# Kernel tuning notes

Measured on AMD Instinct MI355X. Metric: run time of the kernel, lower is better.

The kernel has to match this reference:

```python
import jax, jax.numpy as jnp
import numpy as np

N, E, G = 100000, 600000, 64  # nodes, edges, graphs
F_IN, W, EPS = 32, 128, 1e-5


def setup_inputs() -> dict:
    key = jax.random.key(0)
    ks = jax.random.split(key, 16)
    p = lambda k, shape: jax.random.normal(k, shape, dtype=jnp.float32) * 0.1
    z = lambda n: jnp.zeros((n,), jnp.float32)
    o = lambda n: jnp.ones((n,), jnp.float32)
    return {
        "x": jax.random.normal(ks[0], (N, F_IN), dtype=jnp.float32),
        "edge_index": jax.random.randint(ks[1], (2, E), 0, N, dtype=jnp.int32),
        "batch": jnp.sort(jax.random.randint(ks[2], (N,), 0, G, dtype=jnp.int32)),
        # GCNConv layers
        "W1": p(ks[3], (F_IN, W)), "b1": z(W),
        "W2": p(ks[4], (W, W)), "b2": z(W),
        # mlp_first: Linear -> BN -> ReLU -> Linear
        "W3": p(ks[5], (W, W)), "b3": z(W), "g1": o(W), "be1": z(W),
        "W4": p(ks[6], (W, W)), "b4": z(W),
        # mlp: Linear -> BN -> ReLU -> Linear
        "W5": p(ks[7], (W, W // 2)), "b5": z(W // 2), "g2": o(W // 2), "be2": z(W // 2),
        "W6": p(ks[8], (W // 2, 1)), "b6": z(1),
    }


def gcn_conv(x, src, dst, Wt, b):
    # PyG GCNConv with add_self_loops=True: D^-1/2 (A+I) D^-1/2 (x W) + b
    h = x @ Wt  # [N, width]
    deg = jax.ops.segment_sum(jnp.ones(src.shape[0], x.dtype), dst, num_segments=N) + 1.0
    dinv = jax.lax.rsqrt(deg)
    norm = dinv[src] * dinv[dst]  # per-edge normalization
    agg = jax.ops.segment_sum(h[src] * norm[:, None], dst, num_segments=N)
    # self-loop term: norm for (i,i) is 1/deg[i]
    return agg + h * (dinv * dinv)[:, None] + b


def batch_norm(x, g, b):
    # training-mode BatchNorm1d (batch stats, biased var)
    mu = x.mean(axis=0)
    var = jnp.mean((x - mu) ** 2, axis=0)
    return (x - mu) * jax.lax.rsqrt(var + EPS) * g + b


def reference(x, edge_index, batch, W1, b1, W2, b2, W3, b3, g1, be1, W4, b4, W5, b5, g2, be2, W6, b6):
    src, dst = edge_index[0], edge_index[1]
    x = jax.nn.relu(gcn_conv(x, src, dst, W1, b1))
    x = jax.nn.relu(gcn_conv(x, src, dst, W2, b2))
    # mlp_first + ReLU
    x = jax.nn.relu(batch_norm(x @ W3 + b3, g1, be1)) @ W4 + b4
    x = jax.nn.relu(x)
    # global max pool over nodes per graph
    x = jax.ops.segment_max(x, batch, num_segments=G)  # [G, width]
    # final mlp
    x = jax.nn.relu(batch_norm(x @ W5 + b5, g2, be2)) @ W6 + b6
    return x[:, 0]
```

## Files before the change

kernel.cpp:

```cpp
#include <hip/hip_runtime.h>

#define N_NODES 100000
#define N_EDGES 600000
#define N_GRAPHS 64
#define EPS 1e-5f
#define SCAN_BLOCKS 391

typedef unsigned short u16;
typedef unsigned int u32;
typedef __attribute__((ext_vector_type(8))) short bf16x8;
typedef __attribute__((ext_vector_type(4))) float f32x4;

__device__ __forceinline__ float bf2f(u16 u) { return __uint_as_float(((u32)u) << 16); }
__device__ __forceinline__ u16 f2bf(float f) {
    u32 u = __float_as_uint(f);
    u += 0x7FFFu + ((u >> 16) & 1u);
    return (u16)(u >> 16);
}
__device__ __forceinline__ float2 bfx2(u32 v) {
    float2 r;
    r.x = __uint_as_float(v << 16);
    r.y = __uint_as_float(v & 0xFFFF0000u);
    return r;
}

#define WS_COUNTS   ((size_t)0)
#define WS_CURSOR   ((size_t)400384)
#define WS_POOLED   ((size_t)800768)
#define WS_BNSUM    ((size_t)833536)
#define WS_BNSUMSQ  ((size_t)834048)
#define WS_FLAG     ((size_t)834560)
#define ZERO_BYTES  ((size_t)835072)
#define WS_OFFSETS  ((size_t)835072)
#define WS_DINV     ((size_t)1235456)
#define WS_DINV2    ((size_t)1635840)
#define WS_SRCS     ((size_t)2036224)
#define WS_ZF       ((size_t)4436736)
#define WS_CANONW   ((size_t)4453120)
#define WS_BUFA     ((size_t)4578560)
#define WS_BUFB     ((size_t)30178560)

#define CW_W1 0
#define CW_B1 4096
#define CW_W2 4224
#define CW_B2 20608
#define CW_W3 20736
#define CW_B3 37120
#define CW_G1 37248
#define CW_BE1 37376
#define CW_W4 37504
#define CW_B4 53888
#define CW_W5 54016
#define CW_B5 62208
#define CW_G2 62272
#define CW_BE2 62336
#define CW_W6 62400
#define CW_B6 62464

__global__ void detect_kernel(const u32* __restrict__ xraw, int* __restrict__ flag) {
    __shared__ int cnt;
    if (threadIdx.x == 0) cnt = 0;
    __syncthreads();
    int c = 0;
    for (int i = threadIdx.x; i < 2048; i += 256) {
        u32 w = xraw[i];
        float a = fabsf(__uint_as_float((w & 0xFFFFu) << 16));
        if (a == 0.f || (a > 1e-8f && a < 1e4f)) c++;
    }
    atomicAdd(&cnt, c);
    __syncthreads();
    if (threadIdx.x == 0) *flag = (cnt > 1024) ? 1 : 0;
}

__global__ void convx_kernel(const void* __restrict__ xsrc, u16* __restrict__ dst,
                             const int* __restrict__ flag) {
    int i = blockIdx.x * 256 + threadIdx.x;
    if (i < N_NODES * 32)
        dst[i] = (*flag) ? ((const u16*)xsrc)[i] : f2bf(((const float*)xsrc)[i]);
}

struct SmallArgs {
    const void* src[16];
    int n[16];
    int off[16];
    int cols[16];
};
__global__ void convs_kernel(SmallArgs a, u16* __restrict__ dst, const int* __restrict__ flag) {
    int i = blockIdx.x * 256 + threadIdx.x;
    int isbf = *flag;
#pragma unroll
    for (int j = 0; j < 16; j++)
        if (i < a.n[j]) {
            u16 v = isbf ? ((const u16*)a.src[j])[i] : f2bf(((const float*)a.src[j])[i]);
            if (a.cols[j] > 0) {
                int k = i / a.cols[j];
                int n = i - k * a.cols[j];
                int Kd = a.n[j] / a.cols[j];
                dst[a.off[j] + n * Kd + k] = v;
            } else {
                dst[a.off[j] + i] = v;
            }
        }
}

__global__ void deg_kernel(const int* __restrict__ dst, int* __restrict__ counts) {
    int e = blockIdx.x * 256 + threadIdx.x;
    if (e < N_EDGES) atomicAdd(&counts[dst[e]], 1);
}

__global__ __launch_bounds__(256) void reduce_kernel(const int* __restrict__ counts,
                                                     int* __restrict__ partials) {
    int i = blockIdx.x * 256 + threadIdx.x;
    int v = (i < N_NODES) ? counts[i] : 0;
    for (int off = 32; off > 0; off >>= 1) v += __shfl_down(v, off, 64);
    __shared__ int wsum[4];
    if ((threadIdx.x & 63) == 0) wsum[threadIdx.x >> 6] = v;
    __syncthreads();
    if (threadIdx.x == 0) partials[blockIdx.x] = wsum[0] + wsum[1] + wsum[2] + wsum[3];
}

__global__ __launch_bounds__(512) void scanpart_kernel(int* __restrict__ partials) {
    __shared__ int sc[512];
    int t = threadIdx.x;
    int v = (t < SCAN_BLOCKS) ? partials[t] : 0;
    sc[t] = v;
    __syncthreads();
    for (int off = 1; off < 512; off <<= 1) {
        int u = (t >= off) ? sc[t - off] : 0;
        __syncthreads();
        sc[t] += u;
        __syncthreads();
    }
    if (t < SCAN_BLOCKS) partials[t] = sc[t] - v;
}

__global__ __launch_bounds__(256) void offsets_kernel(const int* __restrict__ counts,
                                                      const int* __restrict__ partials,
                                                      int* __restrict__ offs) {
    int i = blockIdx.x * 256 + threadIdx.x;
    int lane = threadIdx.x & 63, wv = threadIdx.x >> 6;
    int v = (i < N_NODES) ? counts[i] : 0;
    int sv = v;
    for (int off = 1; off < 64; off <<= 1) {
        int u = __shfl_up(sv, off, 64);
        if (lane >= off) sv += u;
    }
    __shared__ int wsum[4];
    if (lane == 63) wsum[wv] = sv;
    __syncthreads();
    int wpre = 0;
    for (int w = 0; w < wv; w++) wpre += wsum[w];
    int excl = sv - v + wpre + partials[blockIdx.x];
    if (i < N_NODES) offs[i] = excl;
    if (i == N_NODES - 1) offs[N_NODES] = excl + v;
}

__global__ void dinv_kernel(const int* __restrict__ counts, float* __restrict__ dinv,
                            float* __restrict__ dinv2) {
    int i = blockIdx.x * 256 + threadIdx.x;
    if (i < N_NODES) {
        float d = (float)(counts[i] + 1);
        float r = rsqrtf(d);
        dinv[i] = r;
        dinv2[i] = r * r;
    }
}

__global__ void scatter_kernel(const int* __restrict__ src, const int* __restrict__ dst,
                               const int* __restrict__ offs, int* __restrict__ cursor,
                               int* __restrict__ srcs) {
    int e = blockIdx.x * 256 + threadIdx.x;
    if (e < N_EDGES) {
        int d = dst[e];
        int p = offs[d] + atomicAdd(&cursor[d], 1);
        srcs[p] = src[e];
    }
}

template <int K, int IN_MODE, int OUT_MODE>
__global__ __launch_bounds__(256, 4) void mgemm_kernel(
    const u16* __restrict__ A, const u16* __restrict__ Wt, const u16* __restrict__ bias,
    u16* __restrict__ C, const float* __restrict__ scl, const float* __restrict__ shf,
    const float* __restrict__ dscale, float* __restrict__ bn_sum,
    float* __restrict__ bn_sumsq, const int* __restrict__ batch, u32* __restrict__ pooled,
    int M) {
    constexpr int KP = K + 8;
    __shared__ __align__(16) u16 Wl[128 * KP];
    __shared__ float csum[128], csumsq[128];

    const int tid = threadIdx.x;
    const int wave = tid >> 6;
    const int lane = tid & 63;
    const int l15 = lane & 15;
    const int quad = lane >> 4;
    const int row0 = blockIdx.x * 128 + wave * 32;

    {
        const u32* g = (const u32*)Wt;
        u32* l = (u32*)Wl;
        for (int i = tid; i < 128 * (K / 2); i += 256) {
            int n = i / (K / 2), j = i - n * (K / 2);
            l[n * (KP / 2) + j] = g[i];
        }
    }
    if (OUT_MODE == 1 && tid < 128) { csum[tid] = 0.f; csumsq[tid] = 0.f; }
    __syncthreads();

    f32x4 acc[2][8];
#pragma unroll
    for (int rt = 0; rt < 2; rt++)
#pragma unroll
        for (int nt = 0; nt < 8; nt++) acc[rt][nt] = {0.f, 0.f, 0.f, 0.f};

#pragma unroll
    for (int k0 = 0; k0 < K; k0 += 32) {
        float s8[8], h8[8];
        if (IN_MODE == 1) {
#pragma unroll
            for (int t = 0; t < 8; t++) {
                s8[t] = scl[k0 + quad * 8 + t];
                h8[t] = shf[k0 + quad * 8 + t];
            }
        }
        bf16x8 af[2];
#pragma unroll
        for (int rt = 0; rt < 2; rt++) {
            int r = row0 + rt * 16 + l15;
            r = min(r, M - 1);
            const u16* p = A + (size_t)r * K + k0 + quad * 8;
            if (IN_MODE == 0) {
                af[rt] = *(const bf16x8*)p;
            } else {
                uint4 raw = *(const uint4*)p;
                u32 w4[4] = {raw.x, raw.y, raw.z, raw.w};
                bf16x8 tmp;
#pragma unroll
                for (int t = 0; t < 4; t++) {
                    float2 f = bfx2(w4[t]);
                    f.x = fmaxf(fmaf(f.x, s8[2 * t], h8[2 * t]), 0.f);
                    f.y = fmaxf(fmaf(f.y, s8[2 * t + 1], h8[2 * t + 1]), 0.f);
                    tmp[2 * t] = (short)f2bf(f.x);
                    tmp[2 * t + 1] = (short)f2bf(f.y);
                }
                af[rt] = tmp;
            }
        }
#pragma unroll
        for (int nt = 0; nt < 8; nt++) {
            bf16x8 bf = *(const bf16x8*)&Wl[(nt * 16 + l15) * KP + k0 + quad * 8];
            acc[0][nt] = __builtin_amdgcn_mfma_f32_16x16x32_bf16(af[0], bf, acc[0][nt], 0, 0, 0);
            acc[1][nt] = __builtin_amdgcn_mfma_f32_16x16x32_bf16(af[1], bf, acc[1][nt], 0, 0, 0);
        }
    }

    if (OUT_MODE == 0) {
#pragma unroll
        for (int rt = 0; rt < 2; rt++)
#pragma unroll
            for (int i = 0; i < 4; i++) {
                int r = row0 + rt * 16 + quad * 4 + i;
                if (r < M) {
                    float ds = dscale[r];
                    u16* cp = C + (size_t)r * 128 + l15;
#pragma unroll
                    for (int nt = 0; nt < 8; nt++) cp[nt * 16] = f2bf(acc[rt][nt][i] * ds);
                }
            }
    } else if (OUT_MODE == 1) {
        float b[8], s[8], sq[8];
#pragma unroll
        for (int nt = 0; nt < 8; nt++) {
            b[nt] = bf2f(bias[nt * 16 + l15]);
            s[nt] = 0.f;
            sq[nt] = 0.f;
        }
#pragma unroll
        for (int rt = 0; rt < 2; rt++)
#pragma unroll
            for (int i = 0; i < 4; i++) {
                int r = row0 + rt * 16 + quad * 4 + i;
                if (r < M) {
                    u16* cp = C + (size_t)r * 128 + l15;
#pragma unroll
                    for (int nt = 0; nt < 8; nt++) {
                        float v = acc[rt][nt][i] + b[nt];
                        s[nt] += v;
                        sq[nt] += v * v;
                        cp[nt * 16] = f2bf(v);
                    }
                }
            }
#pragma unroll
        for (int nt = 0; nt < 8; nt++) {
            atomicAdd(&csum[nt * 16 + l15], s[nt]);
            atomicAdd(&csumsq[nt * 16 + l15], sq[nt]);
        }
        __syncthreads();
        if (tid < 128) {
            atomicAdd(&bn_sum[tid], csum[tid]);
            atomicAdd(&bn_sumsq[tid], csumsq[tid]);
        }
    } else {
        float b[8];
#pragma unroll
        for (int nt = 0; nt < 8; nt++) b[nt] = bf2f(bias[nt * 16 + l15]);
        float cur[8];
#pragma unroll
        for (int nt = 0; nt < 8; nt++) cur[nt] = 0.f;
        int curg = -1;
#pragma unroll
        for (int rt = 0; rt < 2; rt++)
#pragma unroll
            for (int i = 0; i < 4; i++) {
                int r = row0 + rt * 16 + quad * 4 + i;
                if (r < M) {
                    int g = batch[r];
                    if (g != curg) {
                        if (curg >= 0) {
                            u32* bp = pooled + curg * 128 + l15;
#pragma unroll
                            for (int nt = 0; nt < 8; nt++)
                                if (cur[nt] > 0.f)
                                    atomicMax(&bp[nt * 16], __float_as_uint(cur[nt]));
                        }
                        curg = g;
#pragma unroll
                        for (int nt = 0; nt < 8; nt++) cur[nt] = 0.f;
                    }
#pragma unroll
                    for (int nt = 0; nt < 8; nt++)
                        cur[nt] = fmaxf(cur[nt], fmaxf(acc[rt][nt][i] + b[nt], 0.f));
                }
            }
        if (curg >= 0) {
            u32* bp = pooled + curg * 128 + l15;
#pragma unroll
            for (int nt = 0; nt < 8; nt++)
                if (cur[nt] > 0.f) atomicMax(&bp[nt * 16], __float_as_uint(cur[nt]));
        }
    }
}

__global__ __launch_bounds__(256) void conv_kernel(const u16* __restrict__ hs,
                                                   const int* __restrict__ srcs,
                                                   const int* __restrict__ offs,
                                                   const float* __restrict__ dinv,
                                                   const u16* __restrict__ bias,
                                                   u16* __restrict__ xout) {
    int wid = (blockIdx.x * 256 + threadIdx.x) >> 6;
    int lane = threadIdx.x & 63;
    if (wid >= N_NODES) return;
    int l = lane & 15, g = lane >> 4;
    int e0 = offs[wid], e1 = offs[wid + 1];
    float acc[8] = {0.f, 0.f, 0.f, 0.f, 0.f, 0.f, 0.f, 0.f};
    for (int e = e0 + g; e < e1; e += 4) {
        int s = srcs[e];
        uint4 raw = *(const uint4*)(hs + (size_t)s * 128 + l * 8);
        u32 w[4] = {raw.x, raw.y, raw.z, raw.w};
#pragma unroll
        for (int t = 0; t < 4; t++) {
            float2 f = bfx2(w[t]);
            acc[2 * t] += f.x;
            acc[2 * t + 1] += f.y;
        }
    }
#pragma unroll
    for (int j = 0; j < 8; j++) {
        acc[j] += __shfl_xor(acc[j], 16, 64);
        acc[j] += __shfl_xor(acc[j], 32, 64);
    }
    if (g == 0) {
        float di = dinv[wid];
        uint4 own = *(const uint4*)(hs + (size_t)wid * 128 + l * 8);
        uint4 bb = *(const uint4*)(bias + l * 8);
        u32 ow[4] = {own.x, own.y, own.z, own.w};
        u32 bw[4] = {bb.x, bb.y, bb.z, bb.w};
        u32 res[4];
#pragma unroll
        for (int t = 0; t < 4; t++) {
            float2 fo = bfx2(ow[t]);
            float2 fb = bfx2(bw[t]);
            float rx = fmaxf(fmaf(acc[2 * t] + fo.x, di, fb.x), 0.f);
            float ry = fmaxf(fmaf(acc[2 * t + 1] + fo.y, di, fb.y), 0.f);
            res[t] = (u32)f2bf(rx) | ((u32)f2bf(ry) << 16);
        }
        uint4 outp = {res[0], res[1], res[2], res[3]};
        *(uint4*)(xout + (size_t)wid * 128 + l * 8) = outp;
    }
}

__global__ void bnstats_kernel(float* __restrict__ bn_sum, float* __restrict__ bn_sumsq,
                               const u16* __restrict__ g1, const u16* __restrict__ be1) {
    int c = threadIdx.x;
    if (c < 128) {
        float mu = bn_sum[c] / (float)N_NODES;
        float var = bn_sumsq[c] / (float)N_NODES - mu * mu;
        float rstd = rsqrtf(var + EPS);
        float sc = rstd * bf2f(g1[c]);
        bn_sum[c] = sc;
        bn_sumsq[c] = bf2f(be1[c]) - mu * sc;
    }
}

__global__ __launch_bounds__(256) void head1_kernel(const u32* __restrict__ pooled,
                                                    const u16* __restrict__ W5,
                                                    const u16* __restrict__ b5,
                                                    float* __restrict__ zf) {
    __shared__ float red[4][64];
    int g = blockIdx.x;
    int c = threadIdx.x & 63;
    int kq = threadIdx.x >> 6;
    const u32* prow = pooled + g * 128;
    float p = 0.f;
    for (int k = kq * 32; k < kq * 32 + 32; k++)
        p = fmaf(__uint_as_float(prow[k]), bf2f(W5[k * 64 + c]), p);
    red[kq][c] = p;
    __syncthreads();
    if (kq == 0) zf[g * 64 + c] = red[0][c] + red[1][c] + red[2][c] + red[3][c] + bf2f(b5[c]);
}

__global__ __launch_bounds__(64) void head2_kernel(const float* __restrict__ zf,
                                                   const u16* __restrict__ g2,
                                                   const u16* __restrict__ be2,
                                                   const u16* __restrict__ W6,
                                                   const u16* __restrict__ b6,
                                                   void* __restrict__ outv,
                                                   const int* __restrict__ flag) {
    __shared__ float Z[64][65];
    __shared__ float sc[64], sh[64], w6[64];
    int t = threadIdx.x;
    for (int idx = t; idx < 4096; idx += 64) Z[idx >> 6][idx & 63] = zf[idx];
    w6[t] = bf2f(W6[t]);
    __syncthreads();
    {
        float s = 0.f, sq = 0.f;
        for (int g = 0; g < 64; g++) {
            float v = Z[g][t];
            s += v;
            sq += v * v;
        }
        float mu = s * (1.f / 64.f);
        float var = sq * (1.f / 64.f) - mu * mu;
        float rstd = rsqrtf(var + EPS);
        float scale = rstd * bf2f(g2[t]);
        sc[t] = scale;
        sh[t] = bf2f(be2[t]) - mu * scale;
    }
    __syncthreads();
    float o = 0.f;
    for (int c = 0; c < 64; c++)
        o = fmaf(fmaxf(fmaf(Z[t][c], sc[c], sh[c]), 0.f), w6[c], o);
    float res = o + bf2f(b6[0]);
    if (*flag)
        ((u16*)outv)[t] = f2bf(res);
    else
        ((float*)outv)[t] = res;
}

extern "C" void kernel_launch(void* const* d_in, const int* in_sizes, int n_in, void* d_out,
                              int out_size, void* d_ws, size_t ws_size, hipStream_t stream) {
    const void* x = d_in[0];
    const int* ei = (const int*)d_in[1];
    const int* bat = (const int*)d_in[2];

    char* ws = (char*)d_ws;
    int* counts = (int*)(ws + WS_COUNTS);
    int* cursor = (int*)(ws + WS_CURSOR);
    u32* pooled = (u32*)(ws + WS_POOLED);
    float* bnsum = (float*)(ws + WS_BNSUM);
    float* bnssq = (float*)(ws + WS_BNSUMSQ);
    int* flag = (int*)(ws + WS_FLAG);
    int* offs = (int*)(ws + WS_OFFSETS);
    float* dinv = (float*)(ws + WS_DINV);
    float* dinv2 = (float*)(ws + WS_DINV2);
    int* partials = (int*)(ws + WS_DINV2);
    int* srcs = (int*)(ws + WS_SRCS);
    float* zf = (float*)(ws + WS_ZF);
    u16* cw = (u16*)(ws + WS_CANONW);
    u16* bufA = (u16*)(ws + WS_BUFA);
    u16* bufB = (u16*)(ws + WS_BUFB);
    u16* canonx = bufB;

    const int* esrc = ei;
    const int* edst = ei + N_EDGES;

    hipMemsetAsync(ws, 0, ZERO_BYTES, stream);
    detect_kernel<<<1, 256, 0, stream>>>((const u32*)x, flag);

    convx_kernel<<<(N_NODES * 32 + 255) / 256, 256, 0, stream>>>(x, canonx, flag);
    SmallArgs sa;
    const int cw_off[16] = {CW_W1, CW_B1, CW_W2, CW_B2, CW_W3, CW_B3, CW_G1, CW_BE1,
                            CW_W4, CW_B4, CW_W5, CW_B5, CW_G2, CW_BE2, CW_W6, CW_B6};
    const int cw_n[16] = {4096, 128, 16384, 128, 16384, 128, 128, 128,
                          16384, 128, 8192, 64, 64, 64, 64, 1};
    const int cw_c[16] = {128, 0, 128, 0, 128, 0, 0, 0, 128, 0, 0, 0, 0, 0, 0, 0};
    for (int j = 0; j < 16; j++) {
        sa.src[j] = d_in[3 + j];
        sa.n[j] = cw_n[j];
        sa.off[j] = cw_off[j];
        sa.cols[j] = cw_c[j];
    }
    convs_kernel<<<64, 256, 0, stream>>>(sa, cw, flag);

    deg_kernel<<<(N_EDGES + 255) / 256, 256, 0, stream>>>(edst, counts);
    reduce_kernel<<<SCAN_BLOCKS, 256, 0, stream>>>(counts, partials);
    scanpart_kernel<<<1, 512, 0, stream>>>(partials);
    offsets_kernel<<<SCAN_BLOCKS, 256, 0, stream>>>(counts, partials, offs);
    dinv_kernel<<<(N_NODES + 255) / 256, 256, 0, stream>>>(counts, dinv, dinv2);
    scatter_kernel<<<(N_EDGES + 255) / 256, 256, 0, stream>>>(esrc, edst, offs, cursor, srcs);

    const int gb = (N_NODES + 127) / 128;
    const int cb = (N_NODES + 3) / 4;
    mgemm_kernel<32, 0, 0><<<gb, 256, 0, stream>>>(canonx, cw + CW_W1, nullptr, bufA, nullptr,
                                                   nullptr, dinv, nullptr, nullptr, nullptr,
                                                   nullptr, N_NODES);
    conv_kernel<<<cb, 256, 0, stream>>>(bufA, srcs, offs, dinv, cw + CW_B1, bufB);
    mgemm_kernel<128, 0, 0><<<gb, 256, 0, stream>>>(bufB, cw + CW_W2, nullptr, bufA, nullptr,
                                                    nullptr, dinv, nullptr, nullptr, nullptr,
                                                    nullptr, N_NODES);
    conv_kernel<<<cb, 256, 0, stream>>>(bufA, srcs, offs, dinv, cw + CW_B2, bufB);
    mgemm_kernel<128, 0, 1><<<gb, 256, 0, stream>>>(bufB, cw + CW_W3, cw + CW_B3, bufA, nullptr,
                                                    nullptr, nullptr, bnsum, bnssq, nullptr,
                                                    nullptr, N_NODES);
    bnstats_kernel<<<1, 128, 0, stream>>>(bnsum, bnssq, cw + CW_G1, cw + CW_BE1);
    mgemm_kernel<128, 1, 2><<<gb, 256, 0, stream>>>(bufA, cw + CW_W4, cw + CW_B4, nullptr, bnsum,
                                                    bnssq, nullptr, nullptr, nullptr, bat,
                                                    pooled, N_NODES);
    head1_kernel<<<N_GRAPHS, 256, 0, stream>>>(pooled, cw + CW_W5, cw + CW_B5, zf);
    head2_kernel<<<1, 64, 0, stream>>>(zf, cw + CW_G2, cw + CW_BE2, cw + CW_W6, cw + CW_B6,
                                       d_out, flag);
}
```

Before: 381.0 us.

## Load GEMM weights via direct-to-LDS, prefetch A, swap MFMA operands for packed stores

Weight staging in the node GEMM now uses global_load_lds to copy 16-byte fragments straight into LDS in MFMA fragment order, replacing the thread-copied padded layout. All A-row fragments are prefetched into registers before the barrier. For the first three GEMMs the MFMA operands are swapped so each lane holds four consecutive output columns, allowing packed 8-byte stores and a shuffle-based BN column reduction in place of per-lane LDS atomics. Register pressure increases, and launch bounds drop from 4 to 3 waves per SIMD to accommodate it, which may lower occupancy.

```diff
diff --git a/kernel.cpp b/kernel.cpp
--- a/kernel.cpp
+++ b/kernel.cpp
@@ -22,6 +22,10 @@
     r.x = __uint_as_float(v << 16);
     r.y = __uint_as_float(v & 0xFFFF0000u);
     return r;
+}
+__device__ __forceinline__ void load_lds16(const void* g, void* l) {
+    __builtin_amdgcn_global_load_lds((const __attribute__((address_space(1))) void*)g,
+                                     (__attribute__((address_space(3))) void*)l, 16, 0, 0);
 }
 
 #define WS_COUNTS   ((size_t)0)
@@ -177,33 +181,41 @@
     }
 }
 
-template <int K, int IN_MODE, int OUT_MODE>
-__global__ __launch_bounds__(256, 4) void mgemm_kernel(
+template <int K, int IN_MODE, int OUT_MODE, int SWAP>
+__global__ __launch_bounds__(256, 3) void mgemm_kernel(
     const u16* __restrict__ A, const u16* __restrict__ Wt, const u16* __restrict__ bias,
     u16* __restrict__ C, const float* __restrict__ scl, const float* __restrict__ shf,
     const float* __restrict__ dscale, float* __restrict__ bn_sum,
     float* __restrict__ bn_sumsq, const int* __restrict__ batch, u32* __restrict__ pooled,
     int M) {
-    constexpr int KP = K + 8;
-    __shared__ __align__(16) u16 Wl[128 * KP];
+    constexpr int NKT = K / 32;
+    __shared__ __align__(16) u16 Wf[NKT * 8 * 512];
     __shared__ float csum[128], csumsq[128];
 
     const int tid = threadIdx.x;
-    const int wave = tid >> 6;
+    const int wave = __builtin_amdgcn_readfirstlane(tid >> 6);
     const int lane = tid & 63;
     const int l15 = lane & 15;
     const int quad = lane >> 4;
     const int row0 = blockIdx.x * 128 + wave * 32;
 
-    {
-        const u32* g = (const u32*)Wt;
-        u32* l = (u32*)Wl;
-        for (int i = tid; i < 128 * (K / 2); i += 256) {
-            int n = i / (K / 2), j = i - n * (K / 2);
-            l[n * (KP / 2) + j] = g[i];
-        }
+    for (int f = wave; f < NKT * 8; f += 4) {
+        int kt = f >> 3, nt = f & 7;
+        const u16* g = Wt + (nt * 16 + l15) * K + kt * 32 + quad * 8;
+        load_lds16(g, (void*)(Wf + f * 512));
     }
     if (OUT_MODE == 1 && tid < 128) { csum[tid] = 0.f; csumsq[tid] = 0.f; }
+
+    uint4 araw[2][NKT];
+#pragma unroll
+    for (int rt = 0; rt < 2; rt++) {
+        int r = row0 + rt * 16 + l15;
+        r = min(r, M - 1);
+        const u16* p = A + (size_t)r * K + quad * 8;
+#pragma unroll
+        for (int kt = 0; kt < NKT; kt++) araw[rt][kt] = *(const uint4*)(p + kt * 32);
+    }
+
     __syncthreads();
 
     f32x4 acc[2][8];
@@ -213,32 +225,27 @@
         for (int nt = 0; nt < 8; nt++) acc[rt][nt] = {0.f, 0.f, 0.f, 0.f};
 
 #pragma unroll
-    for (int k0 = 0; k0 < K; k0 += 32) {
-        float s8[8], h8[8];
-        if (IN_MODE == 1) {
-#pragma unroll
-            for (int t = 0; t < 8; t++) {
-                s8[t] = scl[k0 + quad * 8 + t];
-                h8[t] = shf[k0 + quad * 8 + t];
-            }
-        }
+    for (int kt = 0; kt < NKT; kt++) {
         bf16x8 af[2];
-#pragma unroll
-        for (int rt = 0; rt < 2; rt++) {
-            int r = row0 + rt * 16 + l15;
-            r = min(r, M - 1);
-            const u16* p = A + (size_t)r * K + k0 + quad * 8;
-            if (IN_MODE == 0) {
-                af[rt] = *(const bf16x8*)p;
-            } else {
-                uint4 raw = *(const uint4*)p;
-                u32 w4[4] = {raw.x, raw.y, raw.z, raw.w};
+        if (IN_MODE == 0) {
+#pragma unroll
+            for (int rt = 0; rt < 2; rt++) af[rt] = __builtin_bit_cast(bf16x8, araw[rt][kt]);
+        } else {
+            float4 sa = *(const float4*)(scl + kt * 32 + quad * 8);
+            float4 sb = *(const float4*)(scl + kt * 32 + quad * 8 + 4);
+            float4 ha = *(const float4*)(shf + kt * 32 + quad * 8);
+            float4 hb = *(const float4*)(shf + kt * 32 + quad * 8 + 4);
+            float se[8] = {sa.x, sa.y, sa.z, sa.w, sb.x, sb.y, sb.z, sb.w};
+            float he[8] = {ha.x, ha.y, ha.z, ha.w, hb.x, hb.y, hb.z, hb.w};
+#pragma unroll
+            for (int rt = 0; rt < 2; rt++) {
+                u32 w4[4] = {araw[rt][kt].x, araw[rt][kt].y, araw[rt][kt].z, araw[rt][kt].w};
                 bf16x8 tmp;
 #pragma unroll
                 for (int t = 0; t < 4; t++) {
                     float2 f = bfx2(w4[t]);
-                    f.x = fmaxf(fmaf(f.x, s8[2 * t], h8[2 * t]), 0.f);
-                    f.y = fmaxf(fmaf(f.y, s8[2 * t + 1], h8[2 * t + 1]), 0.f);
+                    f.x = fmaxf(fmaf(f.x, se[2 * t], he[2 * t]), 0.f);
+                    f.y = fmaxf(fmaf(f.y, se[2 * t + 1], he[2 * t + 1]), 0.f);
                     tmp[2 * t] = (short)f2bf(f.x);
                     tmp[2 * t + 1] = (short)f2bf(f.y);
                 }
@@ -247,54 +254,81 @@
         }
 #pragma unroll
         for (int nt = 0; nt < 8; nt++) {
-            bf16x8 bf = *(const bf16x8*)&Wl[(nt * 16 + l15) * KP + k0 + quad * 8];
-            acc[0][nt] = __builtin_amdgcn_mfma_f32_16x16x32_bf16(af[0], bf, acc[0][nt], 0, 0, 0);
-            acc[1][nt] = __builtin_amdgcn_mfma_f32_16x16x32_bf16(af[1], bf, acc[1][nt], 0, 0, 0);
+            bf16x8 wf = *(const bf16x8*)&Wf[(kt * 8 + nt) * 512 + lane * 8];
+            if (SWAP) {
+                acc[0][nt] = __builtin_amdgcn_mfma_f32_16x16x32_bf16(wf, af[0], acc[0][nt], 0, 0, 0);
+                acc[1][nt] = __builtin_amdgcn_mfma_f32_16x16x32_bf16(wf, af[1], acc[1][nt], 0, 0, 0);
+            } else {
+                acc[0][nt] = __builtin_amdgcn_mfma_f32_16x16x32_bf16(af[0], wf, acc[0][nt], 0, 0, 0);
+                acc[1][nt] = __builtin_amdgcn_mfma_f32_16x16x32_bf16(af[1], wf, acc[1][nt], 0, 0, 0);
+            }
         }
     }
 
     if (OUT_MODE == 0) {
 #pragma unroll
-        for (int rt = 0; rt < 2; rt++)
-#pragma unroll
-            for (int i = 0; i < 4; i++) {
-                int r = row0 + rt * 16 + quad * 4 + i;
-                if (r < M) {
-                    float ds = dscale[r];
-                    u16* cp = C + (size_t)r * 128 + l15;
-#pragma unroll
-                    for (int nt = 0; nt < 8; nt++) cp[nt * 16] = f2bf(acc[rt][nt][i] * ds);
+        for (int rt = 0; rt < 2; rt++) {
+            int r = row0 + rt * 16 + l15;
+            if (r < M) {
+                float ds = dscale[r];
+                u16* cp = C + (size_t)r * 128 + quad * 4;
+#pragma unroll
+                for (int nt = 0; nt < 8; nt++) {
+                    uint2 pk;
+                    pk.x = (u32)f2bf(acc[rt][nt][0] * ds) | ((u32)f2bf(acc[rt][nt][1] * ds) << 16);
+                    pk.y = (u32)f2bf(acc[rt][nt][2] * ds) | ((u32)f2bf(acc[rt][nt][3] * ds) << 16);
+                    *(uint2*)(cp + nt * 16) = pk;
                 }
             }
+        }
     } else if (OUT_MODE == 1) {
-        float b[8], s[8], sq[8];
+        float b[8][4], s[8][4], sq[8][4];
 #pragma unroll
         for (int nt = 0; nt < 8; nt++) {
-            b[nt] = bf2f(bias[nt * 16 + l15]);
-            s[nt] = 0.f;
-            sq[nt] = 0.f;
-        }
-#pragma unroll
-        for (int rt = 0; rt < 2; rt++)
-#pragma unroll
-            for (int i = 0; i < 4; i++) {
-                int r = row0 + rt * 16 + quad * 4 + i;
-                if (r < M) {
-                    u16* cp = C + (size_t)r * 128 + l15;
-#pragma unroll
-                    for (int nt = 0; nt < 8; nt++) {
-                        float v = acc[rt][nt][i] + b[nt];
-                        s[nt] += v;
-                        sq[nt] += v * v;
-                        cp[nt * 16] = f2bf(v);
+            uint2 br = *(const uint2*)(bias + nt * 16 + quad * 4);
+            float2 b01 = bfx2(br.x), b23 = bfx2(br.y);
+            b[nt][0] = b01.x; b[nt][1] = b01.y; b[nt][2] = b23.x; b[nt][3] = b23.y;
+#pragma unroll
+            for (int i = 0; i < 4; i++) { s[nt][i] = 0.f; sq[nt][i] = 0.f; }
+        }
+#pragma unroll
+        for (int rt = 0; rt < 2; rt++) {
+            int r = row0 + rt * 16 + l15;
+            if (r < M) {
+                u16* cp = C + (size_t)r * 128 + quad * 4;
+#pragma unroll
+                for (int nt = 0; nt < 8; nt++) {
+                    float v[4];
+#pragma unroll
+                    for (int i = 0; i < 4; i++) {
+                        v[i] = acc[rt][nt][i] + b[nt][i];
+                        s[nt][i] += v[i];
+                        sq[nt][i] += v[i] * v[i];
                     }
+                    uint2 pk;
+                    pk.x = (u32)f2bf(v[0]) | ((u32)f2bf(v[1]) << 16);
+                    pk.y = (u32)f2bf(v[2]) | ((u32)f2bf(v[3]) << 16);
+                    *(uint2*)(cp + nt * 16) = pk;
                 }
             }
-#pragma unroll
-        for (int nt = 0; nt < 8; nt++) {
-            atomicAdd(&csum[nt * 16 + l15], s[nt]);
-            atomicAdd(&csumsq[nt * 16 + l15], sq[nt]);
-        }
+        }
+#pragma unroll
+        for (int m = 1; m < 16; m <<= 1)
+#pragma unroll
+            for (int nt = 0; nt < 8; nt++)
+#pragma unroll
+                for (int i = 0; i < 4; i++) {
+                    s[nt][i] += __shfl_xor(s[nt][i], m, 64);
+                    sq[nt][i] += __shfl_xor(sq[nt][i], m, 64);
+                }
+        if (l15 == 0)
+#pragma unroll
+            for (int nt = 0; nt < 8; nt++)
+#pragma unroll
+                for (int i = 0; i < 4; i++) {
+                    atomicAdd(&csum[nt * 16 + quad * 4 + i], s[nt][i]);
+                    atomicAdd(&csumsq[nt * 16 + quad * 4 + i], sq[nt][i]);
+                }
         __syncthreads();
         if (tid < 128) {
             atomicAdd(&bn_sum[tid], csum[tid]);
@@ -511,21 +545,21 @@
 
     const int gb = (N_NODES + 127) / 128;
     const int cb = (N_NODES + 3) / 4;
-    mgemm_kernel<32, 0, 0><<<gb, 256, 0, stream>>>(canonx, cw + CW_W1, nullptr, bufA, nullptr,
-                                                   nullptr, dinv, nullptr, nullptr, nullptr,
-                                                   nullptr, N_NODES);
+    mgemm_kernel<32, 0, 0, 1><<<gb, 256, 0, stream>>>(canonx, cw + CW_W1, nullptr, bufA, nullptr,
+                                                      nullptr, dinv, nullptr, nullptr, nullptr,
+                                                      nullptr, N_NODES);
     conv_kernel<<<cb, 256, 0, stream>>>(bufA, srcs, offs, dinv, cw + CW_B1, bufB);
-    mgemm_kernel<128, 0, 0><<<gb, 256, 0, stream>>>(bufB, cw + CW_W2, nullptr, bufA, nullptr,
-                                                    nullptr, dinv, nullptr, nullptr, nullptr,
-                                                    nullptr, N_NODES);
+    mgemm_kernel<128, 0, 0, 1><<<gb, 256, 0, stream>>>(bufB, cw + CW_W2, nullptr, bufA, nullptr,
+                                                       nullptr, dinv, nullptr, nullptr, nullptr,
+                                                       nullptr, N_NODES);
     conv_kernel<<<cb, 256, 0, stream>>>(bufA, srcs, offs, dinv, cw + CW_B2, bufB);
-    mgemm_kernel<128, 0, 1><<<gb, 256, 0, stream>>>(bufB, cw + CW_W3, cw + CW_B3, bufA, nullptr,
-                                                    nullptr, nullptr, bnsum, bnssq, nullptr,
-                                                    nullptr, N_NODES);
+    mgemm_kernel<128, 0, 1, 1><<<gb, 256, 0, stream>>>(bufB, cw + CW_W3, cw + CW_B3, bufA,
+                                                       nullptr, nullptr, nullptr, bnsum, bnssq,
+                                                       nullptr, nullptr, N_NODES);
     bnstats_kernel<<<1, 128, 0, stream>>>(bnsum, bnssq, cw + CW_G1, cw + CW_BE1);
-    mgemm_kernel<128, 1, 2><<<gb, 256, 0, stream>>>(bufA, cw + CW_W4, cw + CW_B4, nullptr, bnsum,
-                                                    bnssq, nullptr, nullptr, nullptr, bat,
-                                                    pooled, N_NODES);
+    mgemm_kernel<128, 1, 2, 0><<<gb, 256, 0, stream>>>(bufA, cw + CW_W4, cw + CW_B4, nullptr,
+                                                       bnsum, bnssq, nullptr, nullptr, nullptr,
+                                                       bat, pooled, N_NODES);
     head1_kernel<<<N_GRAPHS, 256, 0, stream>>>(pooled, cw + CW_W5, cw + CW_B5, zf);
     head2_kernel<<<1, 64, 0, stream>>>(zf, cw + CW_G2, cw + CW_BE2, cw + CW_W6, cw + CW_B6,
                                        d_out, flag);
```

After: 400.3 us. 1.05x slower.

## Fuse GCN neighbor aggregation into following GEMM prologue and merge dinv into offsets

Applied to the files above, without the earlier changes.

Removes the separate conv_kernel and performs the neighbor gather-sum, self term, bias and ReLU inside the next mgemm kernel's prologue (IN_MODE 2), so each lane builds its A fragments in registers directly. This avoids writing and re-reading the aggregated activation buffer and drops two launches. The dinv computation moves into offsets_kernel, and launch bounds drop to 3 blocks per SM to give the fused kernel more registers. The fused gather is now serial per row per lane rather than spread over 4 edge groups per wave, so load-balance and latency hiding on high-degree nodes may suffer.

```diff
diff --git a/kernel.cpp b/kernel.cpp
--- a/kernel.cpp
+++ b/kernel.cpp
@@ -136,7 +136,8 @@
 
 __global__ __launch_bounds__(256) void offsets_kernel(const int* __restrict__ counts,
                                                       const int* __restrict__ partials,
-                                                      int* __restrict__ offs) {
+                                                      int* __restrict__ offs,
+                                                      float* __restrict__ dinv) {
     int i = blockIdx.x * 256 + threadIdx.x;
     int lane = threadIdx.x & 63, wv = threadIdx.x >> 6;
     int v = (i < N_NODES) ? counts[i] : 0;
@@ -151,19 +152,11 @@
     int wpre = 0;
     for (int w = 0; w < wv; w++) wpre += wsum[w];
     int excl = sv - v + wpre + partials[blockIdx.x];
-    if (i < N_NODES) offs[i] = excl;
+    if (i < N_NODES) {
+        offs[i] = excl;
+        dinv[i] = rsqrtf((float)(v + 1));
+    }
     if (i == N_NODES - 1) offs[N_NODES] = excl + v;
-}
-
-__global__ void dinv_kernel(const int* __restrict__ counts, float* __restrict__ dinv,
-                            float* __restrict__ dinv2) {
-    int i = blockIdx.x * 256 + threadIdx.x;
-    if (i < N_NODES) {
-        float d = (float)(counts[i] + 1);
-        float r = rsqrtf(d);
-        dinv[i] = r;
-        dinv2[i] = r * r;
-    }
 }
 
 __global__ void scatter_kernel(const int* __restrict__ src, const int* __restrict__ dst,
@@ -178,13 +171,15 @@
 }
 
 template <int K, int IN_MODE, int OUT_MODE>
-__global__ __launch_bounds__(256, 4) void mgemm_kernel(
+__global__ __launch_bounds__(256, 3) void mgemm_kernel(
     const u16* __restrict__ A, const u16* __restrict__ Wt, const u16* __restrict__ bias,
     u16* __restrict__ C, const float* __restrict__ scl, const float* __restrict__ shf,
     const float* __restrict__ dscale, float* __restrict__ bn_sum,
     float* __restrict__ bn_sumsq, const int* __restrict__ batch, u32* __restrict__ pooled,
-    int M) {
+    const int* __restrict__ goffs, const int* __restrict__ gsrcs,
+    const float* __restrict__ gdinv, const u16* __restrict__ gbias, int M) {
     constexpr int KP = K + 8;
+    constexpr int NKT = K / 32;
     __shared__ __align__(16) u16 Wl[128 * KP];
     __shared__ float csum[128], csumsq[128];
 
@@ -204,6 +199,54 @@
         }
     }
     if (OUT_MODE == 1 && tid < 128) { csum[tid] = 0.f; csumsq[tid] = 0.f; }
+
+    uint4 gr[2][NKT];
+    if (IN_MODE == 2) {
+#pragma unroll
+        for (int rt = 0; rt < 2; rt++) {
+            int r = min(row0 + rt * 16 + l15, M - 1);
+            int e0 = goffs[r], e1 = goffs[r + 1];
+            float ga[NKT][8];
+#pragma unroll
+            for (int kt = 0; kt < NKT; kt++)
+#pragma unroll
+                for (int j = 0; j < 8; j++) ga[kt][j] = 0.f;
+            for (int e = e0; e < e1; e++) {
+                int s = gsrcs[e];
+                const u16* hp = A + (size_t)s * K + quad * 8;
+#pragma unroll
+                for (int kt = 0; kt < NKT; kt++) {
+                    uint4 raw = *(const uint4*)(hp + kt * 32);
+                    u32 w4[4] = {raw.x, raw.y, raw.z, raw.w};
+#pragma unroll
+                    for (int t = 0; t < 4; t++) {
+                        float2 f = bfx2(w4[t]);
+                        ga[kt][2 * t] += f.x;
+                        ga[kt][2 * t + 1] += f.y;
+                    }
+                }
+            }
+            float di = gdinv[r];
+            const u16* op = A + (size_t)r * K + quad * 8;
+#pragma unroll
+            for (int kt = 0; kt < NKT; kt++) {
+                uint4 own = *(const uint4*)(op + kt * 32);
+                uint4 bb = *(const uint4*)(gbias + kt * 32 + quad * 8);
+                u32 ow[4] = {own.x, own.y, own.z, own.w};
+                u32 bw[4] = {bb.x, bb.y, bb.z, bb.w};
+                u32 pk[4];
+#pragma unroll
+                for (int t = 0; t < 4; t++) {
+                    float2 fo = bfx2(ow[t]);
+                    float2 fb = bfx2(bw[t]);
+                    float vx = fmaxf(fmaf(ga[kt][2 * t] + fo.x, di, fb.x), 0.f);
+                    float vy = fmaxf(fmaf(ga[kt][2 * t + 1] + fo.y, di, fb.y), 0.f);
+                    pk[t] = (u32)f2bf(vx) | ((u32)f2bf(vy) << 16);
+                }
+                gr[rt][kt] = {pk[0], pk[1], pk[2], pk[3]};
+            }
+        }
+    }
     __syncthreads();
 
     f32x4 acc[2][8];
@@ -214,24 +257,27 @@
 
 #pragma unroll
     for (int k0 = 0; k0 < K; k0 += 32) {
-        float s8[8], h8[8];
-        if (IN_MODE == 1) {
+        bf16x8 af[2];
+        if (IN_MODE == 2) {
+#pragma unroll
+            for (int rt = 0; rt < 2; rt++) af[rt] = __builtin_bit_cast(bf16x8, gr[rt][k0 / 32]);
+        } else if (IN_MODE == 0) {
+#pragma unroll
+            for (int rt = 0; rt < 2; rt++) {
+                int r = min(row0 + rt * 16 + l15, M - 1);
+                af[rt] = *(const bf16x8*)(A + (size_t)r * K + k0 + quad * 8);
+            }
+        } else {
+            float s8[8], h8[8];
 #pragma unroll
             for (int t = 0; t < 8; t++) {
                 s8[t] = scl[k0 + quad * 8 + t];
                 h8[t] = shf[k0 + quad * 8 + t];
             }
-        }
-        bf16x8 af[2];
-#pragma unroll
-        for (int rt = 0; rt < 2; rt++) {
-            int r = row0 + rt * 16 + l15;
-            r = min(r, M - 1);
-            const u16* p = A + (size_t)r * K + k0 + quad * 8;
-            if (IN_MODE == 0) {
-                af[rt] = *(const bf16x8*)p;
-            } else {
-                uint4 raw = *(const uint4*)p;
+#pragma unroll
+            for (int rt = 0; rt < 2; rt++) {
+                int r = min(row0 + rt * 16 + l15, M - 1);
+                uint4 raw = *(const uint4*)(A + (size_t)r * K + k0 + quad * 8);
                 u32 w4[4] = {raw.x, raw.y, raw.z, raw.w};
                 bf16x8 tmp;
 #pragma unroll
@@ -338,54 +384,6 @@
             for (int nt = 0; nt < 8; nt++)
                 if (cur[nt] > 0.f) atomicMax(&bp[nt * 16], __float_as_uint(cur[nt]));
         }
-    }
-}
-
-__global__ __launch_bounds__(256) void conv_kernel(const u16* __restrict__ hs,
-                                                   const int* __restrict__ srcs,
-                                                   const int* __restrict__ offs,
-                                                   const float* __restrict__ dinv,
-                                                   const u16* __restrict__ bias,
-                                                   u16* __restrict__ xout) {
-    int wid = (blockIdx.x * 256 + threadIdx.x) >> 6;
-    int lane = threadIdx.x & 63;
-    if (wid >= N_NODES) return;
-    int l = lane & 15, g = lane >> 4;
-    int e0 = offs[wid], e1 = offs[wid + 1];
-    float acc[8] = {0.f, 0.f, 0.f, 0.f, 0.f, 0.f, 0.f, 0.f};
-    for (int e = e0 + g; e < e1; e += 4) {
-        int s = srcs[e];
-        uint4 raw = *(const uint4*)(hs + (size_t)s * 128 + l * 8);
-        u32 w[4] = {raw.x, raw.y, raw.z, raw.w};
-#pragma unroll
-        for (int t = 0; t < 4; t++) {
-            float2 f = bfx2(w[t]);
-            acc[2 * t] += f.x;
-            acc[2 * t + 1] += f.y;
-        }
-    }
-#pragma unroll
-    for (int j = 0; j < 8; j++) {
-        acc[j] += __shfl_xor(acc[j], 16, 64);
-        acc[j] += __shfl_xor(acc[j], 32, 64);
-    }
-    if (g == 0) {
-        float di = dinv[wid];
-        uint4 own = *(const uint4*)(hs + (size_t)wid * 128 + l * 8);
-        uint4 bb = *(const uint4*)(bias + l * 8);
-        u32 ow[4] = {own.x, own.y, own.z, own.w};
-        u32 bw[4] = {bb.x, bb.y, bb.z, bb.w};
-        u32 res[4];
-#pragma unroll
-        for (int t = 0; t < 4; t++) {
-            float2 fo = bfx2(ow[t]);
-            float2 fb = bfx2(bw[t]);
-            float rx = fmaxf(fmaf(acc[2 * t] + fo.x, di, fb.x), 0.f);
-            float ry = fmaxf(fmaf(acc[2 * t + 1] + fo.y, di, fb.y), 0.f);
-            res[t] = (u32)f2bf(rx) | ((u32)f2bf(ry) << 16);
-        }
-        uint4 outp = {res[0], res[1], res[2], res[3]};
-        *(uint4*)(xout + (size_t)wid * 128 + l * 8) = outp;
     }
 }
 
@@ -472,7 +470,6 @@
     int* flag = (int*)(ws + WS_FLAG);
     int* offs = (int*)(ws + WS_OFFSETS);
     float* dinv = (float*)(ws + WS_DINV);
-    float* dinv2 = (float*)(ws + WS_DINV2);
     int* partials = (int*)(ws + WS_DINV2);
     int* srcs = (int*)(ws + WS_SRCS);
     float* zf = (float*)(ws + WS_ZF);
@@ -505,27 +502,27 @@
     deg_kernel<<<(N_EDGES + 255) / 256, 256, 0, stream>>>(edst, counts);
     reduce_kernel<<<SCAN_BLOCKS, 256, 0, stream>>>(counts, partials);
     scanpart_kernel<<<1, 512, 0, stream>>>(partials);
-    offsets_kernel<<<SCAN_BLOCKS, 256, 0, stream>>>(counts, partials, offs);
-    dinv_kernel<<<(N_NODES + 255) / 256, 256, 0, stream>>>(counts, dinv, dinv2);
+    offsets_kernel<<<SCAN_BLOCKS, 256, 0, stream>>>(counts, partials, offs, dinv);
     scatter_kernel<<<(N_EDGES + 255) / 256, 256, 0, stream>>>(esrc, edst, offs, cursor, srcs);
 
     const int gb = (N_NODES + 127) / 128;
-    const int cb = (N_NODES + 3) / 4;
     mgemm_kernel<32, 0, 0><<<gb, 256, 0, stream>>>(canonx, cw + CW_W1, nullptr, bufA, nullptr,
                                                    nullptr, dinv, nullptr, nullptr, nullptr,
-                                                   nullptr, N_NODES);
-    conv_kernel<<<cb, 256, 0, stream>>>(bufA, srcs, offs, dinv, cw + CW_B1, bufB);
-    mgemm_kernel<128, 0, 0><<<gb, 256, 0, stream>>>(bufB, cw + CW_W2, nullptr, bufA, nullptr,
+                                                   nullptr, nullptr, nullptr, nullptr, nullptr,
+                                                   N_NODES);
+    mgemm_kernel<128, 2, 0><<<gb, 256, 0, stream>>>(bufA, cw + CW_W2, nullptr, bufB, nullptr,
                                                     nullptr, dinv, nullptr, nullptr, nullptr,
-                                                    nullptr, N_NODES);
-    conv_kernel<<<cb, 256, 0, stream>>>(bufA, srcs, offs, dinv, cw + CW_B2, bufB);
-    mgemm_kernel<128, 0, 1><<<gb, 256, 0, stream>>>(bufB, cw + CW_W3, cw + CW_B3, bufA, nullptr,
+                                                    nullptr, offs, srcs, dinv, cw + CW_B1,
+                                                    N_NODES);
+    mgemm_kernel<128, 2, 1><<<gb, 256, 0, stream>>>(bufB, cw + CW_W3, cw + CW_B3, bufA, nullptr,
                                                     nullptr, nullptr, bnsum, bnssq, nullptr,
-                                                    nullptr, N_NODES);
+                                                    nullptr, offs, srcs, dinv, cw + CW_B2,
+                                                    N_NODES);
     bnstats_kernel<<<1, 128, 0, stream>>>(bnsum, bnssq, cw + CW_G1, cw + CW_BE1);
     mgemm_kernel<128, 1, 2><<<gb, 256, 0, stream>>>(bufA, cw + CW_W4, cw + CW_B4, nullptr, bnsum,
                                                     bnssq, nullptr, nullptr, nullptr, bat,
-                                                    pooled, N_NODES);
+                                                    pooled, nullptr, nullptr, nullptr, nullptr,
+                                                    N_NODES);
     head1_kernel<<<N_GRAPHS, 256, 0, stream>>>(pooled, cw + CW_W5, cw + CW_B5, zf);
     head2_kernel<<<1, 64, 0, stream>>>(zf, cw + CW_G2, cw + CW_BE2, cw + CW_W6, cw + CW_B6,
                                        d_out, flag);
```

Result: faster. 366.1 us (-3.9%).
